# Kernel tuning notes

Measured on AMD Instinct MI355X. Metric: run time of the kernel, lower is better.

Reference implementation:

```python
import jax, jax.numpy as jnp
import numpy as np

N, E, F, H, C = 50000, 800000, 128, 128, 40


def gcn_conv(x, edge_index, W, b):
    """PyG-style GCNConv: add self-loops, symmetric normalization, scatter-add."""
    n = x.shape[0]
    loop = jnp.arange(n, dtype=edge_index.dtype)
    src = jnp.concatenate([edge_index[0], loop])  # [E+N] source nodes
    dst = jnp.concatenate([edge_index[1], loop])  # [E+N] target nodes
    deg = jax.ops.segment_sum(jnp.ones_like(src, dtype=x.dtype), dst, num_segments=n)
    dinv = jnp.where(deg > 0, jax.lax.rsqrt(jnp.maximum(deg, 1e-12)), 0.0)
    norm = dinv[src] * dinv[dst]                  # [E+N]
    h = x @ W                                     # [N, out]
    msg = h[src] * norm[:, None]                  # [E+N, out]
    return jax.ops.segment_sum(msg, dst, num_segments=n) + b


def setup_inputs() -> dict:
    key = jax.random.key(0)
    ks = jax.random.split(key, 8)
    x = jax.random.normal(ks[0], (N, F), dtype=jnp.float32)
    edge_index = jax.random.randint(ks[1], (2, E), 0, N, dtype=jnp.int32)
    s = lambda fan_in: 1.0 / np.sqrt(fan_in)
    W1 = jax.random.normal(ks[2], (F, H), dtype=jnp.float32) * s(F)
    b1 = jax.random.normal(ks[3], (H,), dtype=jnp.float32) * 0.01
    W2 = jax.random.normal(ks[4], (H, C), dtype=jnp.float32) * s(H)
    b2 = jax.random.normal(ks[5], (C,), dtype=jnp.float32) * 0.01
    Wlin = jax.random.normal(ks[6], (C, C), dtype=jnp.float32) * s(C)
    blin = jax.random.normal(ks[7], (C,), dtype=jnp.float32) * 0.01
    return {"x": x, "edge_index": edge_index, "W1": W1, "b1": b1,
            "W2": W2, "b2": b2, "Wlin": Wlin, "blin": blin}


def reference(x, edge_index, W1, b1, W2, b2, Wlin, blin):
    h1 = jax.nn.relu(gcn_conv(x, edge_index, W1, b1))
    h2 = jax.nn.relu(gcn_conv(h1, edge_index, W2, b2))
    out = h2 @ Wlin + blin
    return (h2, out)
```

## Files before the change

### kernel.cpp

```cpp
#include <hip/hip_runtime.h>


constexpr int FDIM = 128;
constexpr int CDIM = 40;
constexpr int NPB  = 64;
constexpr int MAXNB = 1024;
constexpr int CH   = 4096;

typedef _Float16 h8  __attribute__((ext_vector_type(8)));
typedef _Float16 h4  __attribute__((ext_vector_type(4)));
typedef _Float16 h2v __attribute__((ext_vector_type(2)));
typedef float    f4  __attribute__((ext_vector_type(4)));

static inline size_t AL512(size_t x) { return (x + 511) & ~size_t(511); }

__global__ __launch_bounds__(256) void k_bhist(const int* __restrict__ dst,
        int* __restrict__ bcnt, int E, int nb) {
    __shared__ int h[MAXNB];
    for (int i = threadIdx.x; i < nb; i += 256) h[i] = 0;
    __syncthreads();
    for (int i = blockIdx.x * 256 + threadIdx.x; i < E; i += gridDim.x * 256)
        atomicAdd(&h[dst[i] >> 6], 1);
    __syncthreads();
    for (int i = threadIdx.x; i < nb; i += 256) {
        int c = h[i];
        if (c) atomicAdd(&bcnt[i], c);
    }
}

__global__ __launch_bounds__(1024) void k_bscan(const int* __restrict__ bcnt,
        int* __restrict__ bbase, int* __restrict__ bcur, int nb, int E) {
    __shared__ int tmp[1024];
    int t = threadIdx.x;
    int v = (t < nb) ? bcnt[t] : 0;
    tmp[t] = v;
    __syncthreads();
    for (int o = 1; o < 1024; o <<= 1) {
        int u = (t >= o) ? tmp[t - o] : 0;
        __syncthreads();
        tmp[t] += u;
        __syncthreads();
    }
    if (t < nb) { int b = tmp[t] - v; bbase[t] = b; bcur[t] = b; }
    if (t == 0) bbase[nb] = E;
}

__global__ __launch_bounds__(256) void k_partition(const int* __restrict__ src,
        const int* __restrict__ dst, int* __restrict__ bcur,
        unsigned* __restrict__ eb, int E, int nb) {
    __shared__ int hcnt[MAXNB];
    __shared__ int gb[MAXNB];
    int e0 = blockIdx.x * CH;
    int cnt = min(CH, E - e0);
    for (int i = threadIdx.x; i < nb; i += 256) hcnt[i] = 0;
    __syncthreads();
    for (int i = threadIdx.x; i < cnt; i += 256)
        atomicAdd(&hcnt[dst[e0 + i] >> 6], 1);
    __syncthreads();
    for (int i = threadIdx.x; i < nb; i += 256) {
        int c = hcnt[i];
        if (c) gb[i] = atomicAdd(&bcur[i], c);
        hcnt[i] = 0;
    }
    __syncthreads();
    for (int i = threadIdx.x; i < cnt; i += 256) {
        int d = dst[e0 + i], b = d >> 6;
        int p = atomicAdd(&hcnt[b], 1);
        eb[gb[b] + p] = ((unsigned)src[e0 + i] << 6) | (unsigned)(d & 63);
    }
}

__global__ __launch_bounds__(256) void k_bucket_csr(const unsigned* __restrict__ eb,
        const int* __restrict__ bbase, int* __restrict__ offs,
        float* __restrict__ dinv, int* __restrict__ ss, int n) {
    __shared__ int cnt[NPB];
    __shared__ int cur[NPB];
    int b = blockIdx.x;
    int beg = bbase[b], end = bbase[b + 1];
    if (threadIdx.x < NPB) cnt[threadIdx.x] = 0;
    __syncthreads();
    for (int i = beg + threadIdx.x; i < end; i += 256)
        atomicAdd(&cnt[eb[i] & 63], 1);
    __syncthreads();
    if (threadIdx.x < NPB) {
        int v = cnt[threadIdx.x];
        int s = v;
#pragma unroll
        for (int o = 1; o < NPB; o <<= 1) {
            int u = __shfl_up(s, o, 64);
            if (threadIdx.x >= (unsigned)o) s += u;
        }
        int e0 = beg + s - v;
        cur[threadIdx.x] = e0;
        int node = b * NPB + threadIdx.x;
        if (node < n) {
            offs[node] = e0;
            dinv[node] = rsqrtf((float)v + 1.0f);
        }
    }
    __syncthreads();
    for (int i = beg + threadIdx.x; i < end; i += 256) {
        unsigned p = eb[i];
        int pos = atomicAdd(&cur[p & 63], 1);
        ss[pos] = (int)(p >> 6);
    }
}

__global__ __launch_bounds__(256) void k_prep(const float* __restrict__ W1,
        const float* __restrict__ W2, _Float16* __restrict__ W1t,
        _Float16* __restrict__ W2t) {
    int i = blockIdx.x * 256 + threadIdx.x;
    if (i < 128 * 128) {
        int c = i >> 7, k = i & 127;
        W1t[c * 128 + k] = (_Float16)W1[k * 128 + c];
    }
    int j = i - 128 * 128;
    if (j >= 0 && j < 48 * 128) {
        int c = j >> 7, k = j & 127;
        W2t[c * 128 + k] = (c < CDIM) ? (_Float16)W2[k * CDIM + c] : (_Float16)0.f;
    }
}

__global__ __launch_bounds__(256) void k_gemm1(const float* __restrict__ X,
        const _Float16* __restrict__ W1t, const float* __restrict__ dinv,
        _Float16* __restrict__ Hp, int n) {
    __shared__ _Float16 xh[64][136];
    __shared__ _Float16 wt[128][136];
    int t = threadIdx.x;
    int r0 = blockIdx.x * 64;
    for (int i = t; i < 64 * 32; i += 256) {
        int r = i >> 5, c4 = (i & 31) * 4;
        int gr = r0 + r;
        float4 v = make_float4(0.f, 0.f, 0.f, 0.f);
        if (gr < n) v = *(const float4*)&X[(size_t)gr * 128 + c4];
        h4 hv; hv[0] = (_Float16)v.x; hv[1] = (_Float16)v.y;
               hv[2] = (_Float16)v.z; hv[3] = (_Float16)v.w;
        *(h4*)&xh[r][c4] = hv;
    }
    for (int i = t; i < 128 * 16; i += 256) {
        int r = i >> 4, c8 = (i & 15) * 8;
        *(uint4*)&wt[r][c8] = *(const uint4*)&W1t[r * 128 + c8];
    }
    __syncthreads();
    int wid = t >> 6, lane = t & 63;
    int fr = lane & 15, fg = lane >> 4;
    f4 acc[8];
#pragma unroll
    for (int ct = 0; ct < 8; ++ct) acc[ct] = (f4){0.f, 0.f, 0.f, 0.f};
#pragma unroll
    for (int ks = 0; ks < 4; ++ks) {
        h8 a = *(const h8*)&xh[wid * 16 + fr][ks * 32 + fg * 8];
#pragma unroll
        for (int ct = 0; ct < 8; ++ct) {
            h8 b = *(const h8*)&wt[ct * 16 + fr][ks * 32 + fg * 8];
            acc[ct] = __builtin_amdgcn_mfma_f32_16x16x32_f16(a, b, acc[ct], 0, 0, 0);
        }
    }
    int rbase = r0 + wid * 16 + fg * 4;
    float dv[4];
#pragma unroll
    for (int rg = 0; rg < 4; ++rg) dv[rg] = (rbase + rg < n) ? dinv[rbase + rg] : 0.f;
#pragma unroll
    for (int ct = 0; ct < 8; ++ct)
#pragma unroll
        for (int rg = 0; rg < 4; ++rg) {
            int gr = rbase + rg;
            if (gr < n) Hp[(size_t)gr * 128 + ct * 16 + fr] = (_Float16)(acc[ct][rg] * dv[rg]);
        }
}

__global__ __launch_bounds__(256) void k_agg128(const int* __restrict__ ss,
        const int* __restrict__ offs, const _Float16* __restrict__ hp,
        const float* __restrict__ b1, const float* __restrict__ dinv,
        _Float16* __restrict__ h1, int n, int E) {
    int w = (blockIdx.x * 256 + threadIdx.x) >> 6;
    int lane = threadIdx.x & 63;
    if (w >= n) return;
    int beg = offs[w];
    int end = (w == n - 1) ? E : offs[w + 1];
    const h2v* hpv = (const h2v*)hp;
    h2v sv = hpv[(size_t)w * 64 + lane];
    float ax = (float)sv[0], ay = (float)sv[1];
    int j = beg;
    for (; j + 3 < end; j += 4) {
        int s0 = ss[j], s1 = ss[j + 1], s2 = ss[j + 2], s3 = ss[j + 3];
        h2v a = hpv[(size_t)s0 * 64 + lane];
        h2v b = hpv[(size_t)s1 * 64 + lane];
        h2v c = hpv[(size_t)s2 * 64 + lane];
        h2v d = hpv[(size_t)s3 * 64 + lane];
        ax += ((float)a[0] + (float)b[0]) + ((float)c[0] + (float)d[0]);
        ay += ((float)a[1] + (float)b[1]) + ((float)c[1] + (float)d[1]);
    }
    for (; j < end; ++j) {
        int s = ss[j];
        h2v a = hpv[(size_t)s * 64 + lane];
        ax += (float)a[0];
        ay += (float)a[1];
    }
    float dvv = dinv[w];
    float2 bb = *(const float2*)&b1[2 * lane];
    h2v o;
    o[0] = (_Float16)fmaxf(fmaf(dvv, ax, bb.x), 0.f);
    o[1] = (_Float16)fmaxf(fmaf(dvv, ay, bb.y), 0.f);
    *(h2v*)&h1[(size_t)w * 128 + 2 * lane] = o;
}

__global__ __launch_bounds__(256) void k_gemm2(const _Float16* __restrict__ H1,
        const _Float16* __restrict__ W2t, const float* __restrict__ dinv,
        _Float16* __restrict__ Hp2, int n) {
    __shared__ _Float16 xh[64][136];
    __shared__ _Float16 wt[48][136];
    int t = threadIdx.x;
    int r0 = blockIdx.x * 64;
    for (int i = t; i < 64 * 16; i += 256) {
        int r = i >> 4, c8 = (i & 15) * 8;
        int gr = r0 + r;
        uint4 v = make_uint4(0u, 0u, 0u, 0u);
        if (gr < n) v = *(const uint4*)&H1[(size_t)gr * 128 + c8];
        *(uint4*)&xh[r][c8] = v;
    }
    for (int i = t; i < 48 * 16; i += 256) {
        int r = i >> 4, c8 = (i & 15) * 8;
        *(uint4*)&wt[r][c8] = *(const uint4*)&W2t[r * 128 + c8];
    }
    __syncthreads();
    int wid = t >> 6, lane = t & 63;
    int fr = lane & 15, fg = lane >> 4;
    f4 acc[3];
#pragma unroll
    for (int ct = 0; ct < 3; ++ct) acc[ct] = (f4){0.f, 0.f, 0.f, 0.f};
#pragma unroll
    for (int ks = 0; ks < 4; ++ks) {
        h8 a = *(const h8*)&xh[wid * 16 + fr][ks * 32 + fg * 8];
#pragma unroll
        for (int ct = 0; ct < 3; ++ct) {
            h8 b = *(const h8*)&wt[ct * 16 + fr][ks * 32 + fg * 8];
            acc[ct] = __builtin_amdgcn_mfma_f32_16x16x32_f16(a, b, acc[ct], 0, 0, 0);
        }
    }
    int rbase = r0 + wid * 16 + fg * 4;
    float dv[4];
#pragma unroll
    for (int rg = 0; rg < 4; ++rg) dv[rg] = (rbase + rg < n) ? dinv[rbase + rg] : 0.f;
#pragma unroll
    for (int ct = 0; ct < 3; ++ct)
#pragma unroll
        for (int rg = 0; rg < 4; ++rg) {
            int gr = rbase + rg, gc = ct * 16 + fr;
            if (gr < n && gc < CDIM)
                Hp2[(size_t)gr * CDIM + gc] = (_Float16)(acc[ct][rg] * dv[rg]);
        }
}

__global__ __launch_bounds__(256) void k_agg40(const int* __restrict__ ss,
        const int* __restrict__ offs, const _Float16* __restrict__ hp,
        const float* __restrict__ b2, const float* __restrict__ dinv,
        float* __restrict__ h2out, int n, int E) {
    int w = (blockIdx.x * 256 + threadIdx.x) >> 6;
    int lane = threadIdx.x & 63;
    if (w >= n) return;
    int beg = offs[w];
    int end = (w == n - 1) ? E : offs[w + 1];
    bool act = lane < CDIM;
    float acc = act ? (float)hp[(size_t)w * CDIM + lane] : 0.f;
    int j = beg;
    for (; j + 3 < end; j += 4) {
        int s0 = ss[j], s1 = ss[j + 1], s2 = ss[j + 2], s3 = ss[j + 3];
        if (act) {
            float a = (float)hp[(size_t)s0 * CDIM + lane];
            float b = (float)hp[(size_t)s1 * CDIM + lane];
            float c = (float)hp[(size_t)s2 * CDIM + lane];
            float d = (float)hp[(size_t)s3 * CDIM + lane];
            acc += (a + b) + (c + d);
        }
    }
    for (; j < end; ++j) {
        int s = ss[j];
        if (act) acc += (float)hp[(size_t)s * CDIM + lane];
    }
    if (act) h2out[(size_t)w * CDIM + lane] = fmaxf(fmaf(dinv[w], acc, b2[lane]), 0.f);
}

__global__ __launch_bounds__(256) void k_final(const float* __restrict__ h2,
        const float* __restrict__ Wlin, const float* __restrict__ blin,
        float* __restrict__ lin_out, int n) {
    __shared__ float wl[CDIM * CDIM];
    __shared__ float hs[32 * CDIM];
    int t = threadIdx.x;
    int r0 = blockIdx.x * 32;
    for (int i = t; i < CDIM * CDIM; i += 256) wl[i] = Wlin[i];
    int lim = n * CDIM - r0 * CDIM;
    for (int i = t; i < 32 * CDIM; i += 256)
        hs[i] = (i < lim) ? h2[(size_t)r0 * CDIM + i] : 0.f;
    __syncthreads();
    for (int i = t; i < 32 * CDIM; i += 256) {
        int r = i / CDIM, c = i % CDIM;
        int gr = r0 + r;
        if (gr >= n) continue;
        float acc = blin[c];
#pragma unroll
        for (int k = 0; k < CDIM; ++k) acc = fmaf(hs[r * CDIM + k], wl[k * CDIM + c], acc);
        lin_out[(size_t)gr * CDIM + c] = acc;
    }
}

extern "C" void kernel_launch(void* const* d_in, const int* in_sizes, int n_in,
                              void* d_out, int out_size, void* d_ws, size_t ws_size,
                              hipStream_t stream) {
    const float* x    = (const float*)d_in[0];
    const int*   ei   = (const int*)d_in[1];
    const float* W1   = (const float*)d_in[2];
    const float* b1   = (const float*)d_in[3];
    const float* W2   = (const float*)d_in[4];
    const float* b2   = (const float*)d_in[5];
    const float* Wlin = (const float*)d_in[6];
    const float* blin = (const float*)d_in[7];
    float* out = (float*)d_out;

    const int n = in_sizes[0] / FDIM;
    const int E = in_sizes[1] / 2;
    const int* src = ei;
    const int* dst = ei + E;
    const int nb = (n + NPB - 1) / NPB;

    char* ws = (char*)d_ws;
    size_t off = 0;
    int*       bcnt  = (int*)(ws + off);       off = AL512(off + (size_t)nb * 4);
    int*       bbase = (int*)(ws + off);       off = AL512(off + (size_t)(nb + 1) * 4);
    int*       bcur  = (int*)(ws + off);       off = AL512(off + (size_t)nb * 4);
    unsigned*  eb    = (unsigned*)(ws + off);  off = AL512(off + (size_t)E * 4);
    int*       offs  = (int*)(ws + off);       off = AL512(off + (size_t)n * 4);
    int*       ss    = (int*)(ws + off);       off = AL512(off + (size_t)E * 4);
    float*     dinv  = (float*)(ws + off);     off = AL512(off + (size_t)n * 4);
    _Float16*  W1t   = (_Float16*)(ws + off);  off = AL512(off + (size_t)128 * 128 * 2);
    _Float16*  W2t   = (_Float16*)(ws + off);  off = AL512(off + (size_t)48 * 128 * 2);
    _Float16*  hp1   = (_Float16*)(ws + off);  off = AL512(off + (size_t)n * FDIM * 2);
    _Float16*  h1h   = (_Float16*)(ws + off);  off = AL512(off + (size_t)n * FDIM * 2);
    _Float16*  hp2   = (_Float16*)(ws + off);  off = AL512(off + (size_t)n * CDIM * 2);
    (void)ws_size; (void)n_in; (void)out_size;

    float* h2_out  = out;
    float* lin_out = out + (size_t)n * CDIM;

    k_prep<<<(128 * 128 + 48 * 128 + 255) / 256, 256, 0, stream>>>(W1, W2, W1t, W2t);
    hipMemsetAsync(bcnt, 0, (size_t)nb * 4, stream);
    k_bhist<<<256, 256, 0, stream>>>(dst, bcnt, E, nb);
    k_bscan<<<1, 1024, 0, stream>>>(bcnt, bbase, bcur, nb, E);
    k_partition<<<(E + CH - 1) / CH, 256, 0, stream>>>(src, dst, bcur, eb, E, nb);
    k_bucket_csr<<<nb, 256, 0, stream>>>(eb, bbase, offs, dinv, ss, n);

    k_gemm1<<<(n + 63) / 64, 256, 0, stream>>>(x, W1t, dinv, hp1, n);
    k_agg128<<<(n * 64 + 255) / 256, 256, 0, stream>>>(ss, offs, hp1, b1, dinv, h1h, n, E);

    k_gemm2<<<(n + 63) / 64, 256, 0, stream>>>(h1h, W2t, dinv, hp2, n);
    k_agg40<<<(n * 64 + 255) / 256, 256, 0, stream>>>(ss, offs, hp2, b2, dinv, h2_out, n, E);

    k_final<<<(n + 31) / 32, 256, 0, stream>>>(h2_out, Wlin, blin, lin_out, n);
}
```

Measured before the change: 171.6 us.

## Vectorize aggregation gathers with 16-byte loads and pad layer-2 features to 64

The two aggregation kernels now let each wave handle several edges at once, with each lane loading 8 fp16 values (16 bytes) per neighbour instead of 2 or 1. Partial sums are combined with cross-lane shuffles before the bias and ReLU epilogue. The layer-2 intermediate is padded from 40 to 64 columns, so rows are 128-byte aligned and the GEMM computes an extra zero tile. This is meant to cut the number of gather instructions and improve memory coalescing, at the cost of shuffle reductions, more registers and extra padded storage and traffic.

After: 150.5 us. -12.3%, faster.

```diff
diff --git a/kernel.cpp b/kernel.cpp
--- a/kernel.cpp
+++ b/kernel.cpp
@@ -9,7 +9,6 @@
 
 typedef _Float16 h8  __attribute__((ext_vector_type(8)));
 typedef _Float16 h4  __attribute__((ext_vector_type(4)));
-typedef _Float16 h2v __attribute__((ext_vector_type(2)));
 typedef float    f4  __attribute__((ext_vector_type(4)));
 
 static inline size_t AL512(size_t x) { return (x + 511) & ~size_t(511); }
@@ -115,7 +114,7 @@
         W1t[c * 128 + k] = (_Float16)W1[k * 128 + c];
     }
     int j = i - 128 * 128;
-    if (j >= 0 && j < 48 * 128) {
+    if (j >= 0 && j < 64 * 128) {
         int c = j >> 7, k = j & 127;
         W2t[c * 128 + k] = (c < CDIM) ? (_Float16)W2[k * CDIM + c] : (_Float16)0.f;
     }
@@ -178,38 +177,57 @@
     if (w >= n) return;
     int beg = offs[w];
     int end = (w == n - 1) ? E : offs[w + 1];
-    const h2v* hpv = (const h2v*)hp;
-    h2v sv = hpv[(size_t)w * 64 + lane];
-    float ax = (float)sv[0], ay = (float)sv[1];
+    const h8* hpv = (const h8*)hp;
+    int g = lane >> 4, c = lane & 15;
+    h8 sv = hpv[(size_t)w * 16 + c];
+    float acc[8];
+#pragma unroll
+    for (int i = 0; i < 8; ++i) acc[i] = (g == 0) ? (float)sv[i] : 0.f;
     int j = beg;
-    for (; j + 3 < end; j += 4) {
-        int s0 = ss[j], s1 = ss[j + 1], s2 = ss[j + 2], s3 = ss[j + 3];
-        h2v a = hpv[(size_t)s0 * 64 + lane];
-        h2v b = hpv[(size_t)s1 * 64 + lane];
-        h2v c = hpv[(size_t)s2 * 64 + lane];
-        h2v d = hpv[(size_t)s3 * 64 + lane];
-        ax += ((float)a[0] + (float)b[0]) + ((float)c[0] + (float)d[0]);
-        ay += ((float)a[1] + (float)b[1]) + ((float)c[1] + (float)d[1]);
-    }
-    for (; j < end; ++j) {
-        int s = ss[j];
-        h2v a = hpv[(size_t)s * 64 + lane];
-        ax += (float)a[0];
-        ay += (float)a[1];
-    }
-    float dvv = dinv[w];
-    float2 bb = *(const float2*)&b1[2 * lane];
-    h2v o;
-    o[0] = (_Float16)fmaxf(fmaf(dvv, ax, bb.x), 0.f);
-    o[1] = (_Float16)fmaxf(fmaf(dvv, ay, bb.y), 0.f);
-    *(h2v*)&h1[(size_t)w * 128 + 2 * lane] = o;
+    for (; j + 7 < end; j += 8) {
+        int s0 = ss[j + g];
+        int s1 = ss[j + 4 + g];
+        h8 v0 = hpv[(size_t)s0 * 16 + c];
+        h8 v1 = hpv[(size_t)s1 * 16 + c];
+#pragma unroll
+        for (int i = 0; i < 8; ++i) acc[i] += (float)v0[i] + (float)v1[i];
+    }
+    for (; j < end; j += 4) {
+        int idx = j + g;
+        if (idx < end) {
+            int s = ss[idx];
+            h8 v = hpv[(size_t)s * 16 + c];
+#pragma unroll
+            for (int i = 0; i < 8; ++i) acc[i] += (float)v[i];
+        }
+    }
+#pragma unroll
+    for (int i = 0; i < 8; ++i) {
+        acc[i] += __shfl_xor(acc[i], 16);
+        acc[i] += __shfl_xor(acc[i], 32);
+    }
+    if (lane < 16) {
+        float dvv = dinv[w];
+        const float4 bb0 = *(const float4*)&b1[8 * lane];
+        const float4 bb1 = *(const float4*)&b1[8 * lane + 4];
+        h8 o;
+        o[0] = (_Float16)fmaxf(fmaf(dvv, acc[0], bb0.x), 0.f);
+        o[1] = (_Float16)fmaxf(fmaf(dvv, acc[1], bb0.y), 0.f);
+        o[2] = (_Float16)fmaxf(fmaf(dvv, acc[2], bb0.z), 0.f);
+        o[3] = (_Float16)fmaxf(fmaf(dvv, acc[3], bb0.w), 0.f);
+        o[4] = (_Float16)fmaxf(fmaf(dvv, acc[4], bb1.x), 0.f);
+        o[5] = (_Float16)fmaxf(fmaf(dvv, acc[5], bb1.y), 0.f);
+        o[6] = (_Float16)fmaxf(fmaf(dvv, acc[6], bb1.z), 0.f);
+        o[7] = (_Float16)fmaxf(fmaf(dvv, acc[7], bb1.w), 0.f);
+        *(h8*)&h1[(size_t)w * 128 + 8 * lane] = o;
+    }
 }
 
 __global__ __launch_bounds__(256) void k_gemm2(const _Float16* __restrict__ H1,
         const _Float16* __restrict__ W2t, const float* __restrict__ dinv,
         _Float16* __restrict__ Hp2, int n) {
     __shared__ _Float16 xh[64][136];
-    __shared__ _Float16 wt[48][136];
+    __shared__ _Float16 wt[64][136];
     int t = threadIdx.x;
     int r0 = blockIdx.x * 64;
     for (int i = t; i < 64 * 16; i += 256) {
@@ -219,21 +237,21 @@
         if (gr < n) v = *(const uint4*)&H1[(size_t)gr * 128 + c8];
         *(uint4*)&xh[r][c8] = v;
     }
-    for (int i = t; i < 48 * 16; i += 256) {
+    for (int i = t; i < 64 * 16; i += 256) {
         int r = i >> 4, c8 = (i & 15) * 8;
         *(uint4*)&wt[r][c8] = *(const uint4*)&W2t[r * 128 + c8];
     }
     __syncthreads();
     int wid = t >> 6, lane = t & 63;
     int fr = lane & 15, fg = lane >> 4;
-    f4 acc[3];
-#pragma unroll
-    for (int ct = 0; ct < 3; ++ct) acc[ct] = (f4){0.f, 0.f, 0.f, 0.f};
+    f4 acc[4];
+#pragma unroll
+    for (int ct = 0; ct < 4; ++ct) acc[ct] = (f4){0.f, 0.f, 0.f, 0.f};
 #pragma unroll
     for (int ks = 0; ks < 4; ++ks) {
         h8 a = *(const h8*)&xh[wid * 16 + fr][ks * 32 + fg * 8];
 #pragma unroll
-        for (int ct = 0; ct < 3; ++ct) {
+        for (int ct = 0; ct < 4; ++ct) {
             h8 b = *(const h8*)&wt[ct * 16 + fr][ks * 32 + fg * 8];
             acc[ct] = __builtin_amdgcn_mfma_f32_16x16x32_f16(a, b, acc[ct], 0, 0, 0);
         }
@@ -243,12 +261,11 @@
 #pragma unroll
     for (int rg = 0; rg < 4; ++rg) dv[rg] = (rbase + rg < n) ? dinv[rbase + rg] : 0.f;
 #pragma unroll
-    for (int ct = 0; ct < 3; ++ct)
+    for (int ct = 0; ct < 4; ++ct)
 #pragma unroll
         for (int rg = 0; rg < 4; ++rg) {
-            int gr = rbase + rg, gc = ct * 16 + fr;
-            if (gr < n && gc < CDIM)
-                Hp2[(size_t)gr * CDIM + gc] = (_Float16)(acc[ct][rg] * dv[rg]);
+            int gr = rbase + rg;
+            if (gr < n) Hp2[(size_t)gr * 64 + ct * 16 + fr] = (_Float16)(acc[ct][rg] * dv[rg]);
         }
 }
 
@@ -261,24 +278,52 @@
     if (w >= n) return;
     int beg = offs[w];
     int end = (w == n - 1) ? E : offs[w + 1];
-    bool act = lane < CDIM;
-    float acc = act ? (float)hp[(size_t)w * CDIM + lane] : 0.f;
+    const h8* hpv = (const h8*)hp;
+    int g = lane >> 3, c = lane & 7;
+    h8 sv = hpv[(size_t)w * 8 + c];
+    float acc[8];
+#pragma unroll
+    for (int i = 0; i < 8; ++i) acc[i] = (g == 0) ? (float)sv[i] : 0.f;
     int j = beg;
-    for (; j + 3 < end; j += 4) {
-        int s0 = ss[j], s1 = ss[j + 1], s2 = ss[j + 2], s3 = ss[j + 3];
-        if (act) {
-            float a = (float)hp[(size_t)s0 * CDIM + lane];
-            float b = (float)hp[(size_t)s1 * CDIM + lane];
-            float c = (float)hp[(size_t)s2 * CDIM + lane];
-            float d = (float)hp[(size_t)s3 * CDIM + lane];
-            acc += (a + b) + (c + d);
-        }
-    }
-    for (; j < end; ++j) {
-        int s = ss[j];
-        if (act) acc += (float)hp[(size_t)s * CDIM + lane];
-    }
-    if (act) h2out[(size_t)w * CDIM + lane] = fmaxf(fmaf(dinv[w], acc, b2[lane]), 0.f);
+    for (; j + 15 < end; j += 16) {
+        int s0 = ss[j + g];
+        int s1 = ss[j + 8 + g];
+        h8 v0 = hpv[(size_t)s0 * 8 + c];
+        h8 v1 = hpv[(size_t)s1 * 8 + c];
+#pragma unroll
+        for (int i = 0; i < 8; ++i) acc[i] += (float)v0[i] + (float)v1[i];
+    }
+    for (; j < end; j += 8) {
+        int idx = j + g;
+        if (idx < end) {
+            int s = ss[idx];
+            h8 v = hpv[(size_t)s * 8 + c];
+#pragma unroll
+            for (int i = 0; i < 8; ++i) acc[i] += (float)v[i];
+        }
+    }
+#pragma unroll
+    for (int i = 0; i < 8; ++i) {
+        acc[i] += __shfl_xor(acc[i], 8);
+        acc[i] += __shfl_xor(acc[i], 16);
+        acc[i] += __shfl_xor(acc[i], 32);
+    }
+    if (lane < 5) {
+        float dvv = dinv[w];
+        const float4 bb0 = *(const float4*)&b2[8 * lane];
+        const float4 bb1 = *(const float4*)&b2[8 * lane + 4];
+        float4 r0, r1;
+        r0.x = fmaxf(fmaf(dvv, acc[0], bb0.x), 0.f);
+        r0.y = fmaxf(fmaf(dvv, acc[1], bb0.y), 0.f);
+        r0.z = fmaxf(fmaf(dvv, acc[2], bb0.z), 0.f);
+        r0.w = fmaxf(fmaf(dvv, acc[3], bb0.w), 0.f);
+        r1.x = fmaxf(fmaf(dvv, acc[4], bb1.x), 0.f);
+        r1.y = fmaxf(fmaf(dvv, acc[5], bb1.y), 0.f);
+        r1.z = fmaxf(fmaf(dvv, acc[6], bb1.z), 0.f);
+        r1.w = fmaxf(fmaf(dvv, acc[7], bb1.w), 0.f);
+        *(float4*)&h2out[(size_t)w * CDIM + 8 * lane] = r0;
+        *(float4*)&h2out[(size_t)w * CDIM + 8 * lane + 4] = r1;
+    }
 }
 
 __global__ __launch_bounds__(256) void k_final(const float* __restrict__ h2,
@@ -333,16 +378,16 @@
     int*       ss    = (int*)(ws + off);       off = AL512(off + (size_t)E * 4);
     float*     dinv  = (float*)(ws + off);     off = AL512(off + (size_t)n * 4);
     _Float16*  W1t   = (_Float16*)(ws + off);  off = AL512(off + (size_t)128 * 128 * 2);
-    _Float16*  W2t   = (_Float16*)(ws + off);  off = AL512(off + (size_t)48 * 128 * 2);
+    _Float16*  W2t   = (_Float16*)(ws + off);  off = AL512(off + (size_t)64 * 128 * 2);
     _Float16*  hp1   = (_Float16*)(ws + off);  off = AL512(off + (size_t)n * FDIM * 2);
     _Float16*  h1h   = (_Float16*)(ws + off);  off = AL512(off + (size_t)n * FDIM * 2);
-    _Float16*  hp2   = (_Float16*)(ws + off);  off = AL512(off + (size_t)n * CDIM * 2);
+    _Float16*  hp2   = (_Float16*)(ws + off);  off = AL512(off + (size_t)n * 64 * 2);
     (void)ws_size; (void)n_in; (void)out_size;
 
     float* h2_out  = out;
     float* lin_out = out + (size_t)n * CDIM;
 
-    k_prep<<<(128 * 128 + 48 * 128 + 255) / 256, 256, 0, stream>>>(W1, W2, W1t, W2t);
+    k_prep<<<(128 * 128 + 64 * 128 + 255) / 256, 256, 0, stream>>>(W1, W2, W1t, W2t);
     hipMemsetAsync(bcnt, 0, (size_t)nb * 4, stream);
     k_bhist<<<256, 256, 0, stream>>>(dst, bcnt, E, nb);
     k_bscan<<<1, 1024, 0, stream>>>(bcnt, bbase, bcur, nb, E);
```
